# Optimization experiments

Hardware: AMD Instinct MI355X
Metric: run time of the kernel (lower is better)

The kernel has to match this reference:

```python
import jax, jax.numpy as jnp
import numpy as np

B, N, DIM, H, DH = 2, 2048, 1024, 16, 64
SCALE = 8.0
LN_EPS = 1e-5
L2_EPS = 1e-12


def setup_inputs() -> dict:
    key = jax.random.key(0)
    ks = jax.random.split(key, 6)
    s = 0.02  # keep projections at sane magnitude
    return {
        "x": jax.random.normal(ks[0], (B, N, DIM), dtype=jnp.float32),
        "g": jnp.ones((DIM,), dtype=jnp.float32),
        "b": jnp.zeros((DIM,), dtype=jnp.float32),
        "c_attn_w": jax.random.normal(ks[1], (DIM, 3 * DIM), dtype=jnp.float32) * s,
        "c_attn_b": jax.random.normal(ks[2], (3 * DIM,), dtype=jnp.float32) * s,
        "c_proj_w": jax.random.normal(ks[3], (DIM, DIM), dtype=jnp.float32) * s,
        "c_proj_b": jax.random.normal(ks[4], (DIM,), dtype=jnp.float32) * s,
        "to_out_w": jax.random.normal(ks[5], (DIM, DIM), dtype=jnp.float32) * s,
    }


def _l2norm(t):
    # F.normalize(t, dim=-1): t / max(||t||, eps)
    n = jnp.sqrt(jnp.sum(t * t, axis=-1, keepdims=True))
    return t / jnp.maximum(n, L2_EPS)


def reference(x, g, b, c_attn_w, c_attn_b, c_proj_w, c_proj_b, to_out_w):
    # LayerNorm
    mu = jnp.mean(x, axis=-1, keepdims=True)
    var = jnp.mean(jnp.square(x - mu), axis=-1, keepdims=True)
    y = (x - mu) * jax.lax.rsqrt(var + LN_EPS) * g + b  # [B,N,DIM]

    # GPT2 Conv1D c_attn: y @ W + b, split into q/k/v
    qkv = y @ c_attn_w + c_attn_b  # [B,N,3*DIM]
    q, k, v = jnp.split(qkv, 3, axis=-1)

    def split_heads(t):
        return t.reshape(B, N, H, DH).transpose(0, 2, 1, 3)  # [B,H,N,DH]

    q, k, v = split_heads(q), split_heads(k), split_heads(v)

    # cosine-sim attention: L2-normalize q,k, scaled dot product, causal softmax
    qn, kn = _l2norm(q), _l2norm(k)
    sim = jnp.einsum("bhid,bhjd->bhij", qn, kn) * SCALE  # [B,H,N,N]
    mask_value = -jnp.finfo(sim.dtype).max
    causal = jnp.triu(jnp.ones((N, N), dtype=bool), k=1)
    sim = jnp.where(causal, mask_value, sim)
    attn = jax.nn.softmax(sim, axis=-1)
    o = jnp.einsum("bhij,bhjd->bhid", attn, v)  # [B,H,N,DH]

    o = o.transpose(0, 2, 1, 3).reshape(B, N, DIM)
    o = o @ c_proj_w + c_proj_b          # Conv1D c_proj
    out = o @ to_out_w.T                  # Linear to_out (no bias)
    return out
```

## Files before the change

kernel.cpp:

```cpp
#include <hip/hip_runtime.h>
#include <cstdint>
#include <cstddef>

#define Bb 2
#define Nn 2048
#define DIMM 1024
#define Hh 16
#define DHh 64
#define BH (Bb*Hh)
#define MROWS (Bb*Nn)

typedef __bf16 bf16x8 __attribute__((ext_vector_type(8)));
typedef float f32x4 __attribute__((ext_vector_type(4)));
typedef short s16x4 __attribute__((ext_vector_type(4)));

__device__ __forceinline__ unsigned short f2bf(float f) {
  unsigned u = __float_as_uint(f);
  u += 0x7FFFu + ((u >> 16) & 1u);
  return (unsigned short)(u >> 16);
}
__device__ __forceinline__ unsigned short f2bf_fast(float f) {
  return (unsigned short)((__float_as_uint(f) + 0x8000u) >> 16);
}
__device__ __forceinline__ float bf2f(unsigned short s) {
  return __uint_as_float(((unsigned)s) << 16);
}

#define GLDS16(g, l) __builtin_amdgcn_global_load_lds( \
    (const __attribute__((address_space(1))) void*)(g), \
    (__attribute__((address_space(3))) void*)(l), 16, 0, 0)

__global__ __launch_bounds__(256) void prep_kernel(
    const float* __restrict__ x, const float* __restrict__ g,
    const float* __restrict__ b,
    const float* __restrict__ c_attn_w, const float* __restrict__ c_proj_w,
    const float* __restrict__ to_out_w, const float* __restrict__ c_proj_b,
    unsigned short* __restrict__ y,
    unsigned short* __restrict__ wqkv, unsigned short* __restrict__ wpbf,
    unsigned short* __restrict__ wout, float* __restrict__ bc) {
  int bid = blockIdx.x;
  int t = threadIdx.x;
  if (bid < 4096) {
    int row = bid;
    const float4* xr = (const float4*)(x + (size_t)row * DIMM);
    float4 v = xr[t];
    float s  = v.x + v.y + v.z + v.w;
    float ss = v.x*v.x + v.y*v.y + v.z*v.z + v.w*v.w;
    #pragma unroll
    for (int o = 1; o < 64; o <<= 1) { s += __shfl_xor(s, o); ss += __shfl_xor(ss, o); }
    __shared__ float red[8];
    int wv = t >> 6;
    if ((t & 63) == 0) { red[wv] = s; red[wv + 4] = ss; }
    __syncthreads();
    s  = red[0] + red[1] + red[2] + red[3];
    ss = red[4] + red[5] + red[6] + red[7];
    float mu  = s * (1.0f / DIMM);
    float var = ss * (1.0f / DIMM) - mu * mu;
    float rs  = rsqrtf(var + 1e-5f);
    float4 gv = ((const float4*)g)[t];
    float4 bv = ((const float4*)b)[t];
    ushort4 o4;
    o4.x = f2bf((v.x - mu) * rs * gv.x + bv.x);
    o4.y = f2bf((v.y - mu) * rs * gv.y + bv.y);
    o4.z = f2bf((v.z - mu) * rs * gv.z + bv.z);
    o4.w = f2bf((v.w - mu) * rs * gv.w + bv.w);
    ((ushort4*)y)[(size_t)row * 256 + t] = o4;
  } else if (bid < 7168) {
    __shared__ float tile[32][33];
    int bb = bid - 4096;
    int bx = bb % 96, by = bb / 96;
    int tx = t & 31, ty = t >> 5;
    int x2 = bx * 32 + tx;
    int y0 = by * 32;
    #pragma unroll
    for (int j = 0; j < 32; j += 8)
      tile[ty + j][tx] = c_attn_w[(size_t)(y0 + ty + j) * 3072 + x2];
    __syncthreads();
    int ox  = by * 32 + tx;
    int oy0 = bx * 32;
    #pragma unroll
    for (int j = 0; j < 32; j += 8)
      wqkv[(size_t)(oy0 + ty + j) * 1024 + ox] = f2bf(tile[tx][ty + j]);
  } else if (bid < 9216) {
    bool iswp = bid < 8192;
    int bb = bid - (iswp ? 7168 : 8192);
    const float* in = iswp ? c_proj_w : to_out_w;
    unsigned short* out = iswp ? wpbf : wout;
    int i = (bb * 256 + t) * 4;
    float4 v = *(const float4*)(in + i);
    ushort4 o;
    o.x = f2bf(v.x); o.y = f2bf(v.y); o.z = f2bf(v.z); o.w = f2bf(v.w);
    *(ushort4*)(out + i) = o;
  } else {
    int n = (bid - 9216) * 4 + (t >> 6);
    int lane = t & 63;
    const float4* w = (const float4*)(to_out_w + (size_t)n * DIMM);
    const float4* b4 = (const float4*)c_proj_b;
    float s = 0.0f;
    #pragma unroll
    for (int k = 0; k < 4; k++) {
      float4 wv = w[lane + k * 64], bv = b4[lane + k * 64];
      s += wv.x * bv.x + wv.y * bv.y + wv.z * bv.z + wv.w * bv.w;
    }
    #pragma unroll
    for (int o = 1; o < 64; o <<= 1) s += __shfl_xor(s, o);
    if (lane == 0) bc[n] = s;
  }
}

template <int EPI>
__device__ __forceinline__ void gemm_body(
    const unsigned short* __restrict__ A, const unsigned short* __restrict__ Bt,
    const float* __restrict__ bias,
    unsigned short* __restrict__ obf, float* __restrict__ of32,
    unsigned short* __restrict__ q_std, unsigned short* __restrict__ k_std,
    unsigned short* __restrict__ vt_out,
    int M, int N, int K, int bn, int bm,
    unsigned short* smem) {
  int t = threadIdx.x;
  int lane = t & 63, wv = t >> 6;
  int wm = (wv >> 1) * 32, wn = (wv & 1) * 64;
  int l16 = lane & 15, quad = lane >> 4;

  const unsigned short* Ab = A + (size_t)(bm * 128) * K;
  const unsigned short* Bb2 = Bt + (size_t)(bn * 128) * K;
  int srow = t >> 3;
  int gch = (t & 7) ^ (srow & 7);

  f32x4 acc[2][4] = {};
  const int KT = K >> 6;

  auto stage = [&](int kt_, int b_) {
    unsigned short* dA = smem + b_ * 16384;
    unsigned short* dB = dA + 8192;
    const unsigned short* gA = Ab  + (size_t)srow * K + kt_ * 64 + gch * 8;
    const unsigned short* gB = Bb2 + (size_t)srow * K + kt_ * 64 + gch * 8;
    #pragma unroll
    for (int i = 0; i < 2; i++) {
      GLDS16(gA + (size_t)(64 * i) * K, dA + (size_t)(t + 512 * i) * 8);
      GLDS16(gB + (size_t)(64 * i) * K, dB + (size_t)(t + 512 * i) * 8);
    }
  };

  stage(0, 0);
  if (KT > 1) stage(1, 1);

  for (int kt2 = 0; kt2 < KT; ++kt2) {
    if (kt2 < KT - 1) asm volatile("s_waitcnt vmcnt(4)" ::: "memory");
    else              asm volatile("s_waitcnt vmcnt(0)" ::: "memory");
    __builtin_amdgcn_s_barrier();
    __builtin_amdgcn_sched_barrier(0);
    const unsigned short* sA = smem + (kt2 & 1) * 16384;
    const unsigned short* sB = sA + 8192;
    #pragma unroll
    for (int kk = 0; kk < 2; kk++) {
      int slot = (kk * 4 + quad) ^ (l16 & 7);
      bf16x8 af[2], bfr[4];
      #pragma unroll
      for (int i = 0; i < 2; i++)
        af[i] = *(const bf16x8*)(sA + (size_t)(wm + i * 16 + l16) * 64 + slot * 8);
      #pragma unroll
      for (int j = 0; j < 4; j++)
        bfr[j] = *(const bf16x8*)(sB + (size_t)(wn + j * 16 + l16) * 64 + slot * 8);
      __builtin_amdgcn_s_setprio(1);
      #pragma unroll
      for (int i = 0; i < 2; i++)
        #pragma unroll
        for (int j = 0; j < 4; j++)
          acc[i][j] = __builtin_amdgcn_mfma_f32_16x16x32_bf16(af[i], bfr[j], acc[i][j], 0, 0, 0);
      __builtin_amdgcn_s_setprio(0);
    }
    __builtin_amdgcn_sched_barrier(0);
    __builtin_amdgcn_s_barrier();
    __builtin_amdgcn_sched_barrier(0);
    if (kt2 + 2 < KT) stage(kt2 + 2, kt2 & 1);
  }

  float bvals[4];
  #pragma unroll
  for (int j = 0; j < 4; j++)
    bvals[j] = (EPI == 3) ? 0.0f : bias[bn * 128 + wn + j * 16 + l16];

  if (EPI == 0) {
    int which = bn >> 3;
    if (which < 2) {
      #pragma unroll
      for (int i = 0; i < 2; i++) {
        #pragma unroll
        for (int r = 0; r < 4; r++) {
          int m = bm * 128 + wm + i * 16 + quad * 4 + r;
          float vals[4];
          float ss = 0.0f;
          #pragma unroll
          for (int j = 0; j < 4; j++) {
            vals[j] = acc[i][j][r] + bvals[j];
            ss += vals[j] * vals[j];
          }
          ss += __shfl_xor(ss, 1); ss += __shfl_xor(ss, 2);
          ss += __shfl_xor(ss, 4); ss += __shfl_xor(ss, 8);
          float scale = ((which == 0) ? 11.5415603f : 1.0f) / fmaxf(sqrtf(ss), 1e-12f);
          int bi = m >> 11, ns = m & 2047;
          unsigned short* dst = (which == 0) ? q_std : k_std;
          #pragma unroll
          for (int j = 0; j < 4; j++) {
            int n = bn * 128 + wn + j * 16 + l16;
            int nn2 = n & 1023;
            int h = nn2 >> 6, d = nn2 & 63;
            dst[((size_t)((bi * Hh + h) * Nn + ns)) * DHh + d] = f2bf(vals[j] * scale);
          }
        }
      }
    } else {
      __syncthreads();
      #pragma unroll
      for (int i = 0; i < 2; i++) {
        int mchunk = (wm + i * 16) / 4 + quad;
        #pragma unroll
        for (int j = 0; j < 4; j++) {
          int n_local = wn + j * 16 + l16;
          int sw = mchunk ^ (n_local & 31);
          ushort4 pack;
          pack.x = f2bf(acc[i][j][0] + bvals[j]);
          pack.y = f2bf(acc[i][j][1] + bvals[j]);
          pack.z = f2bf(acc[i][j][2] + bvals[j]);
          pack.w = f2bf(acc[i][j][3] + bvals[j]);
          *(ushort4*)(smem + (size_t)n_local * 128 + sw * 4) = pack;
        }
      }
      __syncthreads();
      int drow = t >> 2, mq = t & 3;
      int h = (bn - 16) * 2 + (drow >> 6);
      int d = drow & 63;
      int bi = bm >> 4;
      int ns0 = (bm * 128) & 2047;
      unsigned short* dst = vt_out + ((size_t)(bi * Hh + h) * DHh + d) * Nn + ns0 + mq * 32;
      #pragma unroll
      for (int cc = 0; cc < 8; cc++) {
        int c0 = mq * 8 + cc;
        int s0 = c0 ^ (drow & 31);
        *(ushort4*)(dst + cc * 4) = *(const ushort4*)(smem + (size_t)drow * 128 + s0 * 4);
      }
    }
  } else {
    #pragma unroll
    for (int i = 0; i < 2; i++) {
      #pragma unroll
      for (int j = 0; j < 4; j++) {
        int n = bn * 128 + wn + j * 16 + l16;
        #pragma unroll
        for (int r = 0; r < 4; r++) {
          int m = bm * 128 + wm + i * 16 + quad * 4 + r;
          float val = acc[i][j][r] + bvals[j];
          if (EPI == 2) of32[(size_t)m * N + n] = val;
          else          obf[(size_t)m * N + n] = f2bf(val);
        }
      }
    }
  }
}

__global__ __launch_bounds__(512, 4) void gemm_qkv_wcomb(
    const unsigned short* __restrict__ y, const unsigned short* __restrict__ wqkv,
    const float* __restrict__ c_attn_b,
    unsigned short* __restrict__ q_std, unsigned short* __restrict__ k_std,
    unsigned short* __restrict__ vt_out,
    const unsigned short* __restrict__ wout, const unsigned short* __restrict__ wpbf,
    unsigned short* __restrict__ wcomb) {
  __shared__ unsigned short smem[32768];
  int bn = blockIdx.x, bm = blockIdx.y;
  if (bn < 24) {
    gemm_body<0>(y, wqkv, c_attn_b, nullptr, nullptr, q_std, k_std, vt_out,
                 MROWS, 3 * DIMM, DIMM, bn, bm, smem);
  } else {
    int idx = (bn - 24) * 32 + bm;
    gemm_body<3>(wout, wpbf, nullptr, wcomb, nullptr, nullptr, nullptr, nullptr,
                 DIMM, DIMM, DIMM, idx & 7, idx >> 3, smem);
  }
}

__global__ __launch_bounds__(512, 4) void gemm_final(
    const unsigned short* __restrict__ A, const unsigned short* __restrict__ Bt,
    const float* __restrict__ bias, float* __restrict__ of32) {
  __shared__ unsigned short smem[32768];
  gemm_body<2>(A, Bt, bias, nullptr, of32, nullptr, nullptr, nullptr,
               MROWS, DIMM, DIMM, blockIdx.x, blockIdx.y, smem);
}

__global__ __launch_bounds__(512, 4) void attn_kernel(
    const unsigned short* __restrict__ qn, const unsigned short* __restrict__ kn,
    const unsigned short* __restrict__ vt, unsigned short* __restrict__ o_flat) {
  __shared__ float smemf[16384];
  int t = threadIdx.x, lane = t & 63, wv = t >> 6;
  int half = wv >> 2, strip = wv & 3;
  int l16 = lane & 15, quad = lane >> 4;
  int id = blockIdx.x;
  int qb = (id < 256) ? (15 - (id >> 5)) : ((id - 256) >> 5);
  int bh = id & 31;
  int m0 = qb * 128 + strip * 32;
  const unsigned short* qbase = qn + (size_t)bh * Nn * DHh;
  const unsigned short* kbase = kn + (size_t)bh * Nn * DHh;
  const unsigned short* vbase = vt + (size_t)bh * DHh * Nn;

  bf16x8 aq[2][2];
  #pragma unroll
  for (int i2 = 0; i2 < 2; i2++)
    #pragma unroll
    for (int kk = 0; kk < 2; kk++)
      aq[i2][kk] = *(const bf16x8*)(qbase + (size_t)(m0 + i2 * 16 + l16) * DHh + kk * 32 + quad * 8);

  f32x4 accOT[4][2] = {};
  f32x4 denacc[2] = {};
  const s16x4 vones = {(short)0x3F80, (short)0x3F80, (short)0x3F80, (short)0x3F80};

  int tl = t & 255;
  int srow = tl >> 3;
  int gch = (tl & 7) ^ (srow & 7);
  int nh = qb + 1;
  int kt0 = half * nh;

  auto stageT = [&](int kt_, int b_) {
    int jj = (kt0 + kt_) * 64;
    unsigned short* K_ = (unsigned short*)((char*)smemf + half * 32768 + b_ * 16384);
    unsigned short* V_ = K_ + 4096;
    GLDS16(kbase + (size_t)(jj + srow)      * DHh + gch * 8, K_ + (size_t)tl * 8);
    GLDS16(kbase + (size_t)(jj + srow + 32) * DHh + gch * 8, K_ + (size_t)(tl + 256) * 8);
    GLDS16(vbase + (size_t)srow        * Nn + jj + gch * 8, V_ + (size_t)tl * 8);
    GLDS16(vbase + (size_t)(srow + 32) * Nn + jj + gch * 8, V_ + (size_t)(tl + 256) * 8);
  };

  stageT(0, 0);
  if (nh > 1) stageT(1, 1);

  for (int kt = 0; kt < nh; kt++) {
    if (kt < nh - 1) asm volatile("s_waitcnt vmcnt(4)" ::: "memory");
    else             asm volatile("s_waitcnt vmcnt(0)" ::: "memory");
    __builtin_amdgcn_s_barrier();
    __builtin_amdgcn_sched_barrier(0);
    int j0 = (kt0 + kt) * 64;
    unsigned short* myK = (unsigned short*)((char*)smemf + half * 32768 + (kt & 1) * 16384);
    unsigned short* myV = myK + 4096;

    if (j0 <= m0 + 31) {
      f32x4 sc[4][2] = {};
      #pragma unroll
      for (int kk = 0; kk < 2; kk++) {
        int slot = (kk * 4 + quad) ^ (l16 & 7);
        #pragma unroll
        for (int jt = 0; jt < 4; jt++) {
          bf16x8 ak = *(const bf16x8*)(myK + (size_t)(jt * 16 + l16) * 64 + slot * 8);
          #pragma unroll
          for (int i2 = 0; i2 < 2; i2++)
            sc[jt][i2] = __builtin_amdgcn_mfma_f32_16x16x32_bf16(ak, aq[i2][kk], sc[jt][i2], 0, 0, 0);
        }
      }

      bool fullTile = (j0 + 63) <= m0;
      s16x4 pf[4][2];
      #pragma unroll
      for (int jt = 0; jt < 4; jt++) {
        #pragma unroll
        for (int i2 = 0; i2 < 2; i2++) {
          int m = m0 + i2 * 16 + l16;
          #pragma unroll
          for (int r = 0; r < 4; r++) {
            int j = j0 + jt * 16 + quad * 4 + r;
            float e = sc[jt][i2][r] - 11.5415603f;
            float p;
            asm("v_exp_f32 %0, %1" : "=v"(p) : "v"(e));
            if (!fullTile && j > m) p = 0.0f;
            pf[jt][i2][r] = (short)f2bf_fast(p);
          }
        }
      }

      #pragma unroll
      for (int jt = 0; jt < 4; jt++) {
        #pragma unroll
        for (int i2 = 0; i2 < 2; i2++)
          denacc[i2] = __builtin_amdgcn_mfma_f32_16x16x16bf16_1k(vones, pf[jt][i2], denacc[i2], 0, 0, 0);
        #pragma unroll
        for (int dt = 0; dt < 4; dt++) {
          int row = dt * 16 + l16;
          int ch = (jt * 2 + (quad >> 1)) ^ (l16 & 7);
          s16x4 av = *(const s16x4*)(myV + (size_t)row * 64 + ch * 8 + (quad & 1) * 4);
          #pragma unroll
          for (int i2 = 0; i2 < 2; i2++)
            accOT[dt][i2] = __builtin_amdgcn_mfma_f32_16x16x16bf16_1k(av, pf[jt][i2], accOT[dt][i2], 0, 0, 0);
        }
      }
    }

    __builtin_amdgcn_sched_barrier(0);
    __builtin_amdgcn_s_barrier();
    __builtin_amdgcn_sched_barrier(0);
    if (kt + 2 < nh) stageT(kt + 2, kt & 1);
  }

  float den0 = denacc[0][0];
  float den1 = denacc[1][0];

  __syncthreads();
  float* scr = smemf + strip * 2176;
  if (half == 1) {
    #pragma unroll
    for (int dt = 0; dt < 4; dt++)
      #pragma unroll
      for (int i2 = 0; i2 < 2; i2++)
        *(f32x4*)(scr + ((size_t)(dt * 2 + i2) * 64 + lane) * 4) = accOT[dt][i2];
    scr[2048 + lane] = den0;
    scr[2048 + 64 + lane] = den1;
  }
  __syncthreads();
  if (half == 0) {
    float dinv[2];
    dinv[0] = 1.0f / (den0 + scr[2048 + lane]);
    dinv[1] = 1.0f / (den1 + scr[2048 + 64 + lane]);
    int bi = bh >> 4, h = bh & 15;
    #pragma unroll
    for (int i2 = 0; i2 < 2; i2++) {
      #pragma unroll
      for (int dt = 0; dt < 4; dt++) {
        f32x4 o = accOT[dt][i2] + *(const f32x4*)(scr + ((size_t)(dt * 2 + i2) * 64 + lane) * 4);
        ushort4 o4;
        o4.x = f2bf(o[0] * dinv[i2]);
        o4.y = f2bf(o[1] * dinv[i2]);
        o4.z = f2bf(o[2] * dinv[i2]);
        o4.w = f2bf(o[3] * dinv[i2]);
        int ns = m0 + i2 * 16 + l16;
        int d0 = dt * 16 + quad * 4;
        *(ushort4*)(o_flat + ((size_t)(bi * Nn + ns)) * DIMM + h * DHh + d0) = o4;
      }
    }
  }
}

extern "C" void kernel_launch(void* const* d_in, const int* in_sizes, int n_in,
                              void* d_out, int out_size, void* d_ws, size_t ws_size,
                              hipStream_t stream) {
  const float* x        = (const float*)d_in[0];
  const float* g        = (const float*)d_in[1];
  const float* b        = (const float*)d_in[2];
  const float* c_attn_w = (const float*)d_in[3];
  const float* c_attn_b = (const float*)d_in[4];
  const float* c_proj_w = (const float*)d_in[5];
  const float* c_proj_b = (const float*)d_in[6];
  const float* to_out_w = (const float*)d_in[7];
  float* out = (float*)d_out;

  char* p = (char*)d_ws;
  unsigned short* y     = (unsigned short*)(p + ((size_t)0  << 20));
  unsigned short* qbuf  = (unsigned short*)(p + ((size_t)8  << 20));
  unsigned short* kbuf  = (unsigned short*)(p + ((size_t)16 << 20));
  unsigned short* vtb   = (unsigned short*)(p + ((size_t)24 << 20));
  unsigned short* wpbf  = (unsigned short*)(p + ((size_t)32 << 20));
  unsigned short* wout  = (unsigned short*)(p + ((size_t)34 << 20));
  unsigned short* wqkv  = (unsigned short*)(p + ((size_t)40 << 20));
  unsigned short* wcomb = (unsigned short*)(p + ((size_t)46 << 20));
  float*          bc    = (float*)        (p + ((size_t)48 << 20));

  prep_kernel<<<9472, 256, 0, stream>>>(x, g, b, c_attn_w, c_proj_w, to_out_w,
                                        c_proj_b, y, wqkv, wpbf, wout, bc);
  gemm_qkv_wcomb<<<dim3(26, MROWS / 128), 512, 0, stream>>>(
      y, wqkv, c_attn_b, qbuf, kbuf, vtb, wout, wpbf, wcomb);
  attn_kernel<<<512, 512, 0, stream>>>(qbuf, kbuf, vtb, y);
  gemm_final<<<dim3(DIMM / 128, MROWS / 128), 512, 0, stream>>>(y, wcomb, bc, out);
}
```

Before: 199.8 us.

## Load attention K/V tiles directly from global memory instead of LDS staging

Removes the double-buffered global-to-LDS staging of K and V tiles, along with its waitcnt and barrier synchronisation, from the attention kernel. Each wave now reads its K and V fragments straight from global memory (relying on the caches) and exits the key loop early once past the causal limit. Shared memory shrinks to what the final reduction needs, which may raise occupancy. In exchange, the loads become redundant per wave and less well coalesced, V reads are strided 8-byte accesses, and global latency is no longer hidden by prefetch.

```diff
diff --git a/kernel.cpp b/kernel.cpp
--- a/kernel.cpp
+++ b/kernel.cpp
@@ -289,7 +289,7 @@
 __global__ __launch_bounds__(512, 4) void attn_kernel(
     const unsigned short* __restrict__ qn, const unsigned short* __restrict__ kn,
     const unsigned short* __restrict__ vt, unsigned short* __restrict__ o_flat) {
-  __shared__ float smemf[16384];
+  __shared__ float smemf[8704];
   int t = threadIdx.x, lane = t & 63, wv = t >> 6;
   int half = wv >> 2, strip = wv & 3;
   int l16 = lane & 15, quad = lane >> 4;
@@ -312,88 +312,57 @@
   f32x4 denacc[2] = {};
   const s16x4 vones = {(short)0x3F80, (short)0x3F80, (short)0x3F80, (short)0x3F80};
 
-  int tl = t & 255;
-  int srow = tl >> 3;
-  int gch = (tl & 7) ^ (srow & 7);
   int nh = qb + 1;
   int kt0 = half * nh;
 
-  auto stageT = [&](int kt_, int b_) {
-    int jj = (kt0 + kt_) * 64;
-    unsigned short* K_ = (unsigned short*)((char*)smemf + half * 32768 + b_ * 16384);
-    unsigned short* V_ = K_ + 4096;
-    GLDS16(kbase + (size_t)(jj + srow)      * DHh + gch * 8, K_ + (size_t)tl * 8);
-    GLDS16(kbase + (size_t)(jj + srow + 32) * DHh + gch * 8, K_ + (size_t)(tl + 256) * 8);
-    GLDS16(vbase + (size_t)srow        * Nn + jj + gch * 8, V_ + (size_t)tl * 8);
-    GLDS16(vbase + (size_t)(srow + 32) * Nn + jj + gch * 8, V_ + (size_t)(tl + 256) * 8);
-  };
-
-  stageT(0, 0);
-  if (nh > 1) stageT(1, 1);
-
   for (int kt = 0; kt < nh; kt++) {
-    if (kt < nh - 1) asm volatile("s_waitcnt vmcnt(4)" ::: "memory");
-    else             asm volatile("s_waitcnt vmcnt(0)" ::: "memory");
-    __builtin_amdgcn_s_barrier();
-    __builtin_amdgcn_sched_barrier(0);
     int j0 = (kt0 + kt) * 64;
-    unsigned short* myK = (unsigned short*)((char*)smemf + half * 32768 + (kt & 1) * 16384);
-    unsigned short* myV = myK + 4096;
-
-    if (j0 <= m0 + 31) {
-      f32x4 sc[4][2] = {};
-      #pragma unroll
-      for (int kk = 0; kk < 2; kk++) {
-        int slot = (kk * 4 + quad) ^ (l16 & 7);
-        #pragma unroll
-        for (int jt = 0; jt < 4; jt++) {
-          bf16x8 ak = *(const bf16x8*)(myK + (size_t)(jt * 16 + l16) * 64 + slot * 8);
-          #pragma unroll
-          for (int i2 = 0; i2 < 2; i2++)
-            sc[jt][i2] = __builtin_amdgcn_mfma_f32_16x16x32_bf16(ak, aq[i2][kk], sc[jt][i2], 0, 0, 0);
+    if (j0 > m0 + 31) break;
+
+    f32x4 sc[4][2] = {};
+    #pragma unroll
+    for (int kk = 0; kk < 2; kk++) {
+      #pragma unroll
+      for (int jt = 0; jt < 4; jt++) {
+        bf16x8 ak = *(const bf16x8*)(kbase + (size_t)(j0 + jt * 16 + l16) * DHh + kk * 32 + quad * 8);
+        #pragma unroll
+        for (int i2 = 0; i2 < 2; i2++)
+          sc[jt][i2] = __builtin_amdgcn_mfma_f32_16x16x32_bf16(ak, aq[i2][kk], sc[jt][i2], 0, 0, 0);
+      }
+    }
+
+    bool fullTile = (j0 + 63) <= m0;
+    s16x4 pf[4][2];
+    #pragma unroll
+    for (int jt = 0; jt < 4; jt++) {
+      #pragma unroll
+      for (int i2 = 0; i2 < 2; i2++) {
+        int m = m0 + i2 * 16 + l16;
+        #pragma unroll
+        for (int r = 0; r < 4; r++) {
+          int j = j0 + jt * 16 + quad * 4 + r;
+          float e = sc[jt][i2][r] - 11.5415603f;
+          float p;
+          asm("v_exp_f32 %0, %1" : "=v"(p) : "v"(e));
+          if (!fullTile && j > m) p = 0.0f;
+          pf[jt][i2][r] = (short)f2bf_fast(p);
         }
       }
-
-      bool fullTile = (j0 + 63) <= m0;
-      s16x4 pf[4][2];
-      #pragma unroll
-      for (int jt = 0; jt < 4; jt++) {
-        #pragma unroll
-        for (int i2 = 0; i2 < 2; i2++) {
-          int m = m0 + i2 * 16 + l16;
-          #pragma unroll
-          for (int r = 0; r < 4; r++) {
-            int j = j0 + jt * 16 + quad * 4 + r;
-            float e = sc[jt][i2][r] - 11.5415603f;
-            float p;
-            asm("v_exp_f32 %0, %1" : "=v"(p) : "v"(e));
-            if (!fullTile && j > m) p = 0.0f;
-            pf[jt][i2][r] = (short)f2bf_fast(p);
-          }
-        }
-      }
-
-      #pragma unroll
-      for (int jt = 0; jt < 4; jt++) {
+    }
+
+    #pragma unroll
+    for (int jt = 0; jt < 4; jt++) {
+      #pragma unroll
+      for (int i2 = 0; i2 < 2; i2++)
+        denacc[i2] = __builtin_amdgcn_mfma_f32_16x16x16bf16_1k(vones, pf[jt][i2], denacc[i2], 0, 0, 0);
+      #pragma unroll
+      for (int dt = 0; dt < 4; dt++) {
+        s16x4 av = *(const s16x4*)(vbase + (size_t)(dt * 16 + l16) * Nn + j0 + jt * 16 + quad * 4);
         #pragma unroll
         for (int i2 = 0; i2 < 2; i2++)
-          denacc[i2] = __builtin_amdgcn_mfma_f32_16x16x16bf16_1k(vones, pf[jt][i2], denacc[i2], 0, 0, 0);
-        #pragma unroll
-        for (int dt = 0; dt < 4; dt++) {
-          int row = dt * 16 + l16;
-          int ch = (jt * 2 + (quad >> 1)) ^ (l16 & 7);
-          s16x4 av = *(const s16x4*)(myV + (size_t)row * 64 + ch * 8 + (quad & 1) * 4);
-          #pragma unroll
-          for (int i2 = 0; i2 < 2; i2++)
-            accOT[dt][i2] = __builtin_amdgcn_mfma_f32_16x16x16bf16_1k(av, pf[jt][i2], accOT[dt][i2], 0, 0, 0);
-        }
-      }
-    }
-
-    __builtin_amdgcn_sched_barrier(0);
-    __builtin_amdgcn_s_barrier();
-    __builtin_amdgcn_sched_barrier(0);
-    if (kt + 2 < nh) stageT(kt + 2, kt & 1);
+          accOT[dt][i2] = __builtin_amdgcn_mfma_f32_16x16x16bf16_1k(av, pf[jt][i2], accOT[dt][i2], 0, 0, 0);
+      }
+    }
   }
 
   float den0 = denacc[0][0];
```

Measured after the change: 256.5 us. +28.4%, slower.
